# Optimization experiments

Measured on AMD Instinct MI355X. Metric: run time of the kernel, lower is better.

The kernel has to match this reference:

```python
import jax, jax.numpy as jnp
import numpy as np

C = 512
HEADS = 4
GROUPS = 32
EPS = 1e-6


def setup_inputs() -> dict:
    key = jax.random.key(0)
    ks = jax.random.split(key, 6)
    s = 1.0 / np.sqrt(C)
    return {
        "x": jax.random.normal(ks[0], (2, C, 64, 64), dtype=jnp.float32),
        "gn_scale": jnp.ones((C,), jnp.float32),
        "gn_bias": jnp.zeros((C,), jnp.float32),
        "wq": jax.random.normal(ks[1], (C, C), jnp.float32) * s,
        "bq": jnp.zeros((C,), jnp.float32),
        "wk": jax.random.normal(ks[2], (C, C), jnp.float32) * s,
        "bk": jnp.zeros((C,), jnp.float32),
        "wv": jax.random.normal(ks[3], (C, C), jnp.float32) * s,
        "bv": jnp.zeros((C,), jnp.float32),
        "wo": jax.random.normal(ks[4], (C, C), jnp.float32) * s,
        "bo": jnp.zeros((C,), jnp.float32),
    }


def group_norm(x, scale, bias):
    # x: [b, c, h, w]; GroupNorm with 32 groups, eps 1e-6, affine
    b, c, h, w = x.shape
    xg = x.reshape(b, GROUPS, c // GROUPS, h, w)
    mean = jnp.mean(xg, axis=(2, 3, 4), keepdims=True)
    var = jnp.var(xg, axis=(2, 3, 4), keepdims=True)
    xg = (xg - mean) * jax.lax.rsqrt(var + EPS)
    x = xg.reshape(b, c, h, w)
    return x * scale[None, :, None, None] + bias[None, :, None, None]


def conv1x1(x, w, b):
    # 1x1 conv == per-pixel linear: [b,c,h,w] x [o,c] -> [b,o,h,w]
    return jnp.einsum('bchw,oc->bohw', x, w) + b[None, :, None, None]


def reference(x, gn_scale, gn_bias, wq, bq, wk, bk, wv, bv, wo, bo):
    b, c, h, w = x.shape
    hc = c // HEADS
    n = h * w

    h_ = group_norm(x, gn_scale, gn_bias)
    q = conv1x1(h_, wq, bq).reshape(b, HEADS, hc, n)
    k = conv1x1(h_, wk, bk).reshape(b, HEADS, hc, n)
    v = conv1x1(h_, wv, bv).reshape(b, HEADS, hc, n)

    # NOTE: scale uses full channel count c (repo quirk), not head_channel
    scale = jnp.asarray(c, x.dtype) ** -0.5
    scores = jnp.einsum('bhcn,bhcm->bhnm', q, k) * scale  # [b,H,N,N]
    attn = jax.nn.softmax(scores, axis=-1)
    out = jnp.einsum('bhnm,bhcm->bhcn', attn, v)  # [b,H,hc,N]

    out = out.reshape(b, c, h, w)
    return x + conv1x1(out, wo, bo)
```

## Files before the change

### kernel.cpp

```cpp
#include <hip/hip_runtime.h>

typedef float    f32x4 __attribute__((ext_vector_type(4)));
typedef short    bf16x8 __attribute__((ext_vector_type(8)));
typedef unsigned short u16;
typedef u16      u16x4 __attribute__((ext_vector_type(4)));
typedef unsigned u32;
typedef u32      u32x4 __attribute__((ext_vector_type(4)));

#define MFMA16(a, b, c) __builtin_amdgcn_mfma_f32_16x16x32_bf16((a), (b), (c), 0, 0, 0)

#define CCH 512
#define NPIX 4096
#define NHEAD 4
#define HC 128
#define NSPLIT 2
#define KVCHUNK (NPIX / NSPLIT)
#define QK_SCALE 0.04419417382415922f
#define LOG2E 1.4426950408889634f

__device__ __forceinline__ u16 f2b(float f) {
  unsigned u = __builtin_bit_cast(unsigned, f);
  u += 0x7FFFu + ((u >> 16) & 1u);
  return (u16)(u >> 16);
}
__device__ __forceinline__ float b2f(u16 b) {
  return __builtin_bit_cast(float, ((unsigned)b) << 16);
}

__device__ __forceinline__ void gl_lds16(const u16* g, u16* l) {
  __builtin_amdgcn_global_load_lds((const __attribute__((address_space(1))) void*)g,
                                   (__attribute__((address_space(3))) void*)l, 16, 0, 0);
}

__global__ void prep_k(const float* __restrict__ w0, const float* __restrict__ w1,
                       const float* __restrict__ w2, const float* __restrict__ w3,
                       u16* __restrict__ dst,
                       const float* __restrict__ x, float* __restrict__ pstats) {
  int blk = blockIdx.x, t = threadIdx.x;
  if (blk < 1024) {
    int m = blk >> 8;
    const float* src = (m == 0) ? w0 : (m == 1) ? w1 : (m == 2) ? w2 : w3;
    int i = ((blk & 255) * 256 + t) * 4;
    f32x4 v = *(const f32x4*)(src + i);
    u16x4 o = { f2b(v[0]), f2b(v[1]), f2b(v[2]), f2b(v[3]) };
    *(u16x4*)(dst + (size_t)m * (CCH * CCH) + i) = o;
    return;
  }
  int sblk = blk - 1024;
  const f32x4* p = (const f32x4*)(x + (size_t)sblk * 4096);
  int wv = t >> 6, l = t & 63;
  float s = 0.f, ss = 0.f;
  #pragma unroll
  for (int i = t; i < 1024; i += 256) {
    f32x4 v = p[i];
    s  += v[0] + v[1] + v[2] + v[3];
    ss += v[0]*v[0] + v[1]*v[1] + v[2]*v[2] + v[3]*v[3];
  }
  #pragma unroll
  for (int d = 32; d; d >>= 1) { s += __shfl_down(s, d, 64); ss += __shfl_down(ss, d, 64); }
  __shared__ float red[8];
  if (l == 0) { red[wv*2] = s; red[wv*2+1] = ss; }
  __syncthreads();
  if (t == 0) {
    pstats[sblk*2]   = red[0] + red[2] + red[4] + red[6];
    pstats[sblk*2+1] = red[1] + red[3] + red[5] + red[7];
  }
}

__global__ void gn_norm_k(const float* __restrict__ x, const float* __restrict__ gns,
                          const float* __restrict__ gnb, const float* __restrict__ pstats,
                          u16* __restrict__ Ht) {
  int t = threadIdx.x;
  int ct = blockIdx.x * 64, nt = blockIdx.y * 64, b = blockIdx.z;
  int c0 = ct + (t & 15) * 4;
  int n0 = nt + (t >> 4) * 4;
  const float* xb = x + ((size_t)b * CCH + c0) * NPIX + n0;
  int g = b * 32 + (c0 >> 4);
  const f32x4* ps = (const f32x4*)(pstats + g * 32);
  float s = 0.f, ss = 0.f;
  #pragma unroll
  for (int j = 0; j < 8; ++j) {
    f32x4 v = ps[j];
    s  += v[0] + v[2];
    ss += v[1] + v[3];
  }
  float mean = s * (1.f/65536.f);
  float var  = ss * (1.f/65536.f) - mean*mean;
  float rstd = rsqrtf(var + 1e-6f);
  f32x4 rows[4];
  #pragma unroll
  for (int j = 0; j < 4; ++j) {
    f32x4 v = *(const f32x4*)(xb + (size_t)j * NPIX);
    float a  = rstd * gns[c0 + j];
    float bb = gnb[c0 + j] - mean * a;
    rows[j] = v * a + bb;
  }
  #pragma unroll
  for (int i = 0; i < 4; ++i) {
    u16x4 o = { f2b(rows[0][i]), f2b(rows[1][i]), f2b(rows[2][i]), f2b(rows[3][i]) };
    *(u16x4*)(Ht + ((size_t)b * NPIX + n0 + i) * CCH + c0) = o;
  }
}

template<int MODE>
__device__ __forceinline__ void gemm_body(const u16* __restrict__ A,
                                          const u16* __restrict__ B,
                                          const float* __restrict__ bias,
                                          const float* __restrict__ bias2,
                                          u16* __restrict__ outb,
                                          u16* __restrict__ outb2,
                                          float alpha,
                                          int bx, int by, int z,
                                          u16* As, u16* Bs) {
  const int t = threadIdx.x, l = t & 63, wv = t >> 6;
  const int l16 = l & 15, lq = l >> 4;
  const int mt = bx * 128, nt = by * 128;
  const u16* Ap = A + (size_t)mt * CCH;
  const u16* Bp = (MODE == 3) ? (B + (size_t)nt * CCH)
                              : (B + ((size_t)z * NPIX + nt) * CCH);
  const int wm = (wv >> 1) * 64, wn = (wv & 1) * 64;
  f32x4 acc[4][4] = {};

  #pragma unroll
  for (int j = 0; j < 2; ++j) {
    int idx = t + j * 256;
    int row = idx >> 2, kc = (idx & 3) * 8;
    gl_lds16(Ap + (size_t)row * CCH + kc, As + idx * 8);
    gl_lds16(Bp + (size_t)row * CCH + kc, Bs + idx * 8);
  }
  asm volatile("s_waitcnt vmcnt(0)" ::: "memory");
  __syncthreads();

#define GEMM_BODY(CUR, K0, DOSTAGE)                                                   \
  {                                                                                   \
    if (DOSTAGE) {                                                                    \
      _Pragma("unroll")                                                               \
      for (int j = 0; j < 2; ++j) {                                                   \
        int idx = t + j * 256;                                                        \
        int row = idx >> 2, kc = (idx & 3) * 8;                                       \
        gl_lds16(Ap + (size_t)row * CCH + (K0) + 32 + kc, As + ((CUR) ^ 1) * 4096 + idx * 8); \
        gl_lds16(Bp + (size_t)row * CCH + (K0) + 32 + kc, Bs + ((CUR) ^ 1) * 4096 + idx * 8); \
      }                                                                               \
    }                                                                                 \
    bf16x8 af[4], bfr[4];                                                             \
    _Pragma("unroll")                                                                 \
    for (int i = 0; i < 4; ++i) {                                                     \
      af[i]  = *(const bf16x8*)(As + (CUR) * 4096 + (wm + i * 16 + l16) * 32 + lq * 8); \
      bfr[i] = *(const bf16x8*)(Bs + (CUR) * 4096 + (wn + i * 16 + l16) * 32 + lq * 8); \
    }                                                                                 \
    _Pragma("unroll")                                                                 \
    for (int mi = 0; mi < 4; ++mi)                                                    \
      _Pragma("unroll")                                                               \
      for (int ni = 0; ni < 4; ++ni)                                                  \
        acc[mi][ni] = MFMA16(af[mi], bfr[ni], acc[mi][ni]);                           \
    asm volatile("s_waitcnt vmcnt(0)" ::: "memory");                                  \
    __syncthreads();                                                                  \
  }

  for (int k0 = 0; k0 < CCH; k0 += 64) {
    GEMM_BODY(0, k0, true)
    GEMM_BODY(1, k0 + 32, (k0 + 64 < CCH))
  }
#undef GEMM_BODY

  #pragma unroll
  for (int mi = 0; mi < 4; ++mi)
    #pragma unroll
    for (int ni = 0; ni < 4; ++ni)
      #pragma unroll
      for (int r = 0; r < 4; ++r) {
        int grow = mt + wm + mi * 16 + lq * 4 + r;
        int gcol = nt + wn + ni * 16 + l16;
        float v = acc[mi][ni][r];
        if (MODE == 1) {
          outb[((size_t)z * CCH + grow) * NPIX + gcol] = f2b(v + bias[grow]);
        } else {
          if (gcol < 512)
            outb[(size_t)grow * CCH + gcol] = f2b((v + bias[gcol]) * alpha);
          else
            outb2[(size_t)grow * CCH + (gcol - 512)] = f2b(v + bias2[gcol - 512]);
        }
      }
}

__global__ __launch_bounds__(256) void qkv_k(const u16* __restrict__ Ht,
                                             const u16* __restrict__ wb,
                                             const float* __restrict__ bq,
                                             const float* __restrict__ bk,
                                             const float* __restrict__ bv,
                                             u16* __restrict__ Qt, u16* __restrict__ Kt,
                                             u16* __restrict__ Vc, float alpha) {
  __shared__ __align__(16) u16 As[2][4096];
  __shared__ __align__(16) u16 Bs[2][4096];
  int blk = blockIdx.x;
  if (blk < 512) {
    gemm_body<3>(Ht, wb, bq, bk, Qt, Kt, alpha, blk & 63, blk >> 6, 0,
                 &As[0][0], &Bs[0][0]);
  } else {
    int r = blk - 512;
    gemm_body<1>(wb + 2u * 262144u, Ht, bv, nullptr, Vc, nullptr, 1.0f,
                 r & 3, (r >> 2) & 31, r >> 7, &As[0][0], &Bs[0][0]);
  }
}

__global__ __launch_bounds__(256, 2) void flash_k(const u16* __restrict__ Qt,
                                                  const u16* __restrict__ Kt,
                                                  const u16* __restrict__ Vc,
                                                  u16* __restrict__ sl0, u16* __restrict__ sl1,
                                                  float* __restrict__ mlp) {
  __shared__ __align__(16) char lds[65536];
  const int t = threadIdx.x, wv = t >> 6, l = t & 63;
  const int l16 = l & 15, lq = l >> 4;
  const int orig = blockIdx.x;
  const int gid = (orig & 7) * 64 + (orig >> 3);
  const int qx = gid & 31, grp = gid >> 5;
  const int hd = grp & 3, b = (grp >> 2) & 1, s = grp >> 3;
  const int qt0 = qx * 128 + wv * 32;

  const u16* Q = Qt + ((size_t)b * NPIX + qt0) * CCH + hd * HC;
  const u16* Kbase = Kt + (size_t)b * NPIX * CCH + hd * HC;
  const u16* Vbase = Vc + (size_t)b * CCH * NPIX + (size_t)hd * HC * NPIX;
  u16* slab = (s == 0) ? sl0 : sl1;
  u16* Ob = slab + ((size_t)(b * NHEAD + hd) * NPIX + qt0) * HC;
  size_t mlR0 = (size_t)s * 32768 + (size_t)(b * NHEAD + hd) * NPIX + qt0;

  bf16x8 qf[2][4];
  #pragma unroll
  for (int mi = 0; mi < 2; ++mi)
    #pragma unroll
    for (int kk = 0; kk < 4; ++kk)
      qf[mi][kk] = *(const bf16x8*)(Q + (size_t)(mi * 16 + l16) * CCH + kk * 32 + lq * 8);

  const int m_beg = s * KVCHUNK;
  const int sw = (l16 & 7) << 4;
  const int vb2 = (lq & 1) * 32 + (lq >> 1) * 16;

  int kbase[4], vbase[2];
  #pragma unroll
  for (int kk = 0; kk < 4; ++kk) kbase[kk] = l16 * 256 + ((kk * 64 + lq * 16) ^ sw);
  #pragma unroll
  for (int ks = 0; ks < 2; ++ks) vbase[ks] = 32768 + l16 * 128 + ((ks * 64 + vb2) ^ sw);

  u32 kgo[4], vgo[4];
  #pragma unroll
  for (int j = 0; j < 4; ++j) {
    int g = j * 256 + t;
    { int row = g >> 4, src = ((g & 15) << 4) ^ ((row & 7) << 4);
      kgo[j] = (u32)row * CCH + (src >> 1); }
    { int row = g >> 3, src = ((g & 7) << 4) ^ ((row & 7) << 4);
      vgo[j] = (u32)row * NPIX + (src >> 1); }
  }

  const short one_bf = (short)0x3F80;
  const bf16x8 vones = { one_bf, one_bf, one_bf, one_bf, one_bf, one_bf, one_bf, one_bf };

  f32x4 oacc[2][8] = {};
  f32x4 osum[2] = {};

  {
    const u16* kg = Kbase + (size_t)m_beg * CCH;
    const u16* vg = Vbase + m_beg;
    #pragma unroll
    for (int j = 0; j < 4; ++j) {
      gl_lds16(kg + kgo[j], (u16*)lds + (j * 256 + t) * 8);
      gl_lds16(vg + vgo[j], (u16*)(lds + 32768) + (j * 256 + t) * 8);
    }
  }
  asm volatile("s_waitcnt vmcnt(0)" ::: "memory");
  __syncthreads();

  const int NT = KVCHUNK / 64;

#define FLASH_BODY(CUR, M0, DOSTAGE)                                                   \
  {                                                                                    \
    if (DOSTAGE) {                                                                     \
      const u16* kg = Kbase + (size_t)((M0) + 64) * CCH;                               \
      const u16* vg = Vbase + ((M0) + 64);                                             \
      _Pragma("unroll")                                                                \
      for (int j = 0; j < 4; ++j) {                                                    \
        gl_lds16(kg + kgo[j], (u16*)(lds + ((CUR) ^ 1) * 16384) + (j * 256 + t) * 8);  \
        gl_lds16(vg + vgo[j], (u16*)(lds + 32768 + ((CUR) ^ 1) * 16384) + (j * 256 + t) * 8); \
      }                                                                                \
    }                                                                                  \
    f32x4 S[2][4] = {};                                                                \
    __builtin_amdgcn_s_setprio(1);                                                     \
    _Pragma("unroll")                                                                  \
    for (int kk = 0; kk < 4; ++kk)                                                     \
      _Pragma("unroll")                                                                \
      for (int mm = 0; mm < 4; ++mm) {                                                 \
        bf16x8 kf = *(const bf16x8*)(lds + kbase[kk] + mm * 4096 + (CUR) * 16384);     \
        S[0][mm] = MFMA16(kf, qf[0][kk], S[0][mm]);                                    \
        S[1][mm] = MFMA16(kf, qf[1][kk], S[1][mm]);                                    \
      }                                                                                \
    __builtin_amdgcn_s_setprio(0);                                                     \
    u32 pk[2][4][2];                                                                   \
    _Pragma("unroll")                                                                  \
    for (int mi = 0; mi < 2; ++mi) {                                                   \
      _Pragma("unroll")                                                                \
      for (int mm = 0; mm < 4; ++mm) {                                                 \
        f32x4 p;                                                                       \
        _Pragma("unroll")                                                              \
        for (int r = 0; r < 4; ++r) p[r] = exp2f(S[mi][mm][r]);                        \
        asm("v_cvt_pk_bf16_f32 %0, %1, %2" : "=v"(pk[mi][mm][0]) : "v"(p[0]), "v"(p[1])); \
        asm("v_cvt_pk_bf16_f32 %0, %1, %2" : "=v"(pk[mi][mm][1]) : "v"(p[2]), "v"(p[3])); \
      }                                                                                \
    }                                                                                  \
    bf16x8 pa[2][2];                                                                   \
    _Pragma("unroll")                                                                  \
    for (int mi = 0; mi < 2; ++mi)                                                     \
      _Pragma("unroll")                                                                \
      for (int ks = 0; ks < 2; ++ks) {                                                 \
        u32 a0 = pk[mi][2 * ks][0], a1 = pk[mi][2 * ks][1];                            \
        u32 b0 = pk[mi][2 * ks + 1][0], b1 = pk[mi][2 * ks + 1][1];                    \
        asm("v_permlane16_swap_b32 %0, %1" : "+v"(a0), "+v"(b0));                      \
        asm("v_permlane16_swap_b32 %0, %1" : "+v"(a1), "+v"(b1));                      \
        u32x4 w = { a0, a1, b0, b1 };                                                  \
        pa[mi][ks] = __builtin_bit_cast(bf16x8, w);                                    \
      }                                                                                \
    __builtin_amdgcn_s_setprio(1);                                                     \
    _Pragma("unroll")                                                                  \
    for (int ks = 0; ks < 2; ++ks) {                                                   \
      osum[0] = MFMA16(pa[0][ks], vones, osum[0]);                                     \
      osum[1] = MFMA16(pa[1][ks], vones, osum[1]);                                     \
      _Pragma("unroll")                                                                \
      for (int cc = 0; cc < 8; ++cc) {                                                 \
        bf16x8 vf = *(const bf16x8*)(lds + vbase[ks] + cc * 2048 + (CUR) * 16384);     \
        oacc[0][cc] = MFMA16(pa[0][ks], vf, oacc[0][cc]);                              \
        oacc[1][cc] = MFMA16(pa[1][ks], vf, oacc[1][cc]);                              \
      }                                                                                \
    }                                                                                  \
    __builtin_amdgcn_s_setprio(0);                                                     \
    asm volatile("s_waitcnt vmcnt(0)" ::: "memory");                                   \
    __syncthreads();                                                                   \
  }

  for (int it = 0; it < NT; it += 2) {
    FLASH_BODY(0, m_beg + it * 64, true)
    FLASH_BODY(1, m_beg + it * 64 + 64, (it + 2 < NT))
  }
#undef FLASH_BODY

  #pragma unroll
  for (int mi = 0; mi < 2; ++mi)
    #pragma unroll
    for (int cc = 0; cc < 8; ++cc)
      #pragma unroll
      for (int r = 0; r < 4; ++r)
        Ob[(size_t)(mi * 16 + lq * 4 + r) * HC + cc * 16 + l16] = f2b(oacc[mi][cc][r]);
  if (l16 == 0) {
    #pragma unroll
    for (int mi = 0; mi < 2; ++mi)
      #pragma unroll
      for (int r = 0; r < 4; ++r)
        mlp[mlR0 + mi * 16 + lq * 4 + r] = osum[mi][r];
  }
}

__global__ __launch_bounds__(256) void fgemm_k(const u16* __restrict__ Wo,
                                               const u16* __restrict__ sl0,
                                               const u16* __restrict__ sl1,
                                               const float* __restrict__ ml,
                                               const float* __restrict__ bias,
                                               const float* __restrict__ resid,
                                               float* __restrict__ outf) {
  __shared__ __align__(16) u16 As[2][4096];
  __shared__ __align__(16) u16 B0[2][2048];
  __shared__ __align__(16) u16 B1[2][2048];
  const int t = threadIdx.x, l = t & 63, wv = t >> 6;
  const int l16 = l & 15, lq = l >> 4;
  const int mt = blockIdx.x * 128, nt = blockIdx.y * 64, z = blockIdx.z;
  const u16* Ap = Wo + (size_t)mt * CCH;
  const int wm = (wv >> 1) * 64, wn = (wv & 1) * 32;

  float lsum[4][2];
  #pragma unroll
  for (int h = 0; h < 4; ++h)
    #pragma unroll
    for (int ni = 0; ni < 2; ++ni) {
      int gcol = nt + wn + ni * 16 + l16;
      int R = ((z * 4 + h) << 12) + gcol;
      lsum[h][ni] = ml[R] + ml[32768 + R];
    }

  f32x4 acc[4][2] = {};

  #pragma unroll
  for (int j = 0; j < 2; ++j) {
    int idx = t + j * 256;
    int row = idx >> 2, kc = (idx & 3) * 8;
    gl_lds16(Ap + (size_t)row * CCH + kc, &As[0][0] + idx * 8);
  }
  {
    int row = t >> 2, kc = (t & 3) * 8;
    size_t srow = ((size_t)(z * 4) * NPIX + nt + row) * HC + kc;
    gl_lds16(sl0 + srow, &B0[0][0] + t * 8);
    gl_lds16(sl1 + srow, &B1[0][0] + t * 8);
  }
  asm volatile("s_waitcnt vmcnt(0)" ::: "memory");
  __syncthreads();

#define FG_BODY(CUR, K0, DOSTAGE)                                                     \
  {                                                                                   \
    if (DOSTAGE) {                                                                    \
      const int kn = (K0) + 32;                                                       \
      const int hn = kn >> 7, cn = kn & 127;                                          \
      _Pragma("unroll")                                                               \
      for (int j = 0; j < 2; ++j) {                                                   \
        int idx = t + j * 256;                                                        \
        int row = idx >> 2, kc = (idx & 3) * 8;                                       \
        gl_lds16(Ap + (size_t)row * CCH + kn + kc, &As[(CUR) ^ 1][0] + idx * 8);      \
      }                                                                               \
      {                                                                               \
        int row = t >> 2, kc = (t & 3) * 8;                                           \
        size_t srow = ((size_t)(z * 4 + hn) * NPIX + nt + row) * HC + cn + kc;        \
        gl_lds16(sl0 + srow, &B0[(CUR) ^ 1][0] + t * 8);                              \
        gl_lds16(sl1 + srow, &B1[(CUR) ^ 1][0] + t * 8);                              \
      }                                                                               \
    }                                                                                 \
    bf16x8 af[4], b0f[2], b1f[2];                                                     \
    _Pragma("unroll")                                                                 \
    for (int i = 0; i < 4; ++i)                                                       \
      af[i]  = *(const bf16x8*)(&As[CUR][0] + (wm + i * 16 + l16) * 32 + lq * 8);     \
    _Pragma("unroll")                                                                 \
    for (int i = 0; i < 2; ++i) {                                                     \
      b0f[i] = *(const bf16x8*)(&B0[CUR][0] + (wn + i * 16 + l16) * 32 + lq * 8);     \
      b1f[i] = *(const bf16x8*)(&B1[CUR][0] + (wn + i * 16 + l16) * 32 + lq * 8);     \
    }                                                                                 \
    _Pragma("unroll")                                                                 \
    for (int mi = 0; mi < 4; ++mi)                                                    \
      _Pragma("unroll")                                                               \
      for (int ni = 0; ni < 2; ++ni) {                                                \
        acc[mi][ni] = MFMA16(af[mi], b0f[ni], acc[mi][ni]);                           \
        acc[mi][ni] = MFMA16(af[mi], b1f[ni], acc[mi][ni]);                           \
      }                                                                               \
    asm volatile("s_waitcnt vmcnt(0)" ::: "memory");                                  \
    __syncthreads();                                                                  \
  }

  #pragma unroll
  for (int h = 0; h < 4; ++h) {
    if (h) {
      #pragma unroll
      for (int ni = 0; ni < 2; ++ni) {
        float rat = lsum[h][ni] / lsum[h - 1][ni];
        #pragma unroll
        for (int mi = 0; mi < 4; ++mi) acc[mi][ni] *= rat;
      }
    }
    FG_BODY(0, h * 128,      true)
    FG_BODY(1, h * 128 + 32, true)
    FG_BODY(0, h * 128 + 64, true)
    FG_BODY(1, h * 128 + 96, (h < 3))
  }
#undef FG_BODY

  #pragma unroll
  for (int ni = 0; ni < 2; ++ni) {
    float inv3 = 1.f / lsum[3][ni];
    int gcol = nt + wn + ni * 16 + l16;
    #pragma unroll
    for (int mi = 0; mi < 4; ++mi)
      #pragma unroll
      for (int r = 0; r < 4; ++r) {
        int grow = mt + wm + mi * 16 + lq * 4 + r;
        size_t off = ((size_t)z * CCH + grow) * NPIX + gcol;
        outf[off] = acc[mi][ni][r] * inv3 + bias[grow] + resid[off];
      }
  }
}

extern "C" void kernel_launch(void* const* d_in, const int* in_sizes, int n_in,
                              void* d_out, int out_size, void* d_ws, size_t ws_size,
                              hipStream_t stream) {
  const float* x   = (const float*)d_in[0];
  const float* gns = (const float*)d_in[1];
  const float* gnb = (const float*)d_in[2];
  const float* wq  = (const float*)d_in[3];
  const float* bq  = (const float*)d_in[4];
  const float* wk  = (const float*)d_in[5];
  const float* bk  = (const float*)d_in[6];
  const float* wv  = (const float*)d_in[7];
  const float* bv  = (const float*)d_in[8];
  const float* wo  = (const float*)d_in[9];
  const float* bo  = (const float*)d_in[10];
  float* out = (float*)d_out;
  char* ws = (char*)d_ws;

  u16*   wb    = (u16*)ws;
  u16*   Ht    = (u16*)(ws + (size_t)( 2u << 20));
  u16*   Qt    = (u16*)(ws + (size_t)(10u << 20));
  u16*   Kt    = (u16*)(ws + (size_t)(18u << 20));
  u16*   Vc    = (u16*)(ws + (size_t)(26u << 20));
  u16*   sl1   = (u16*)(ws + (size_t)(34u << 20));
  float* mlb   = (float*)(ws + (size_t)(42u << 20));
  float* stats = (float*)(ws + (size_t)(43u << 20));
  u16*   sl0   = Ht;

  prep_k    <<<dim3(2048, 1, 1), 256, 0, stream>>>(wq, wk, wv, wo, wb, x, stats);
  gn_norm_k <<<dim3(8, 64, 2),   256, 0, stream>>>(x, gns, gnb, stats, Ht);
  qkv_k     <<<dim3(768, 1, 1),  256, 0, stream>>>(Ht, wb, bq, bk, bv, Qt, Kt, Vc,
                                                   QK_SCALE * LOG2E);
  flash_k   <<<dim3(512, 1, 1),  256, 0, stream>>>(Qt, Kt, Vc, sl0, sl1, mlb);
  fgemm_k   <<<dim3(4, 64, 2),   256, 0, stream>>>(wb + 3u * 262144u, sl0, sl1, mlb,
                                                   bo, x, out);
}
```

Before: 143.1 us.

## Halve QKV GEMM N-tile and flash KV tile to shrink LDS and raise occupancy

The QKV GEMM tile shrinks from 128x128 to 128x64, doubling the grid to 1536 blocks and halving B-side shared memory. The flash attention kernel's KV tile drops from 64 to 32 keys per iteration, halving LDS to 32KB and adjusting the V swizzle and permlane packing to a single k-step. The intent is better occupancy and wave-level parallelism. The cost is more loop iterations with barrier overhead and less operand reuse per tile.

After: 147.9 us. 1.03x slower.

```diff
diff --git a/kernel.cpp b/kernel.cpp
--- a/kernel.cpp
+++ b/kernel.cpp
@@ -114,19 +114,22 @@
                                           u16* As, u16* Bs) {
   const int t = threadIdx.x, l = t & 63, wv = t >> 6;
   const int l16 = l & 15, lq = l >> 4;
-  const int mt = bx * 128, nt = by * 128;
+  const int mt = bx * 128, nt = by * 64;
   const u16* Ap = A + (size_t)mt * CCH;
   const u16* Bp = (MODE == 3) ? (B + (size_t)nt * CCH)
                               : (B + ((size_t)z * NPIX + nt) * CCH);
-  const int wm = (wv >> 1) * 64, wn = (wv & 1) * 64;
-  f32x4 acc[4][4] = {};
+  const int wm = (wv >> 1) * 64, wn = (wv & 1) * 32;
+  f32x4 acc[4][2] = {};
 
   #pragma unroll
   for (int j = 0; j < 2; ++j) {
     int idx = t + j * 256;
     int row = idx >> 2, kc = (idx & 3) * 8;
     gl_lds16(Ap + (size_t)row * CCH + kc, As + idx * 8);
-    gl_lds16(Bp + (size_t)row * CCH + kc, Bs + idx * 8);
+  }
+  {
+    int row = t >> 2, kc = (t & 3) * 8;
+    gl_lds16(Bp + (size_t)row * CCH + kc, Bs + t * 8);
   }
   asm volatile("s_waitcnt vmcnt(0)" ::: "memory");
   __syncthreads();
@@ -139,19 +142,23 @@
         int idx = t + j * 256;                                                        \
         int row = idx >> 2, kc = (idx & 3) * 8;                                       \
         gl_lds16(Ap + (size_t)row * CCH + (K0) + 32 + kc, As + ((CUR) ^ 1) * 4096 + idx * 8); \
-        gl_lds16(Bp + (size_t)row * CCH + (K0) + 32 + kc, Bs + ((CUR) ^ 1) * 4096 + idx * 8); \
+      }                                                                               \
+      {                                                                               \
+        int row = t >> 2, kc = (t & 3) * 8;                                           \
+        gl_lds16(Bp + (size_t)row * CCH + (K0) + 32 + kc, Bs + ((CUR) ^ 1) * 2048 + t * 8); \
       }                                                                               \
     }                                                                                 \
-    bf16x8 af[4], bfr[4];                                                             \
+    bf16x8 af[4], bfr[2];                                                             \
     _Pragma("unroll")                                                                 \
-    for (int i = 0; i < 4; ++i) {                                                     \
+    for (int i = 0; i < 4; ++i)                                                       \
       af[i]  = *(const bf16x8*)(As + (CUR) * 4096 + (wm + i * 16 + l16) * 32 + lq * 8); \
-      bfr[i] = *(const bf16x8*)(Bs + (CUR) * 4096 + (wn + i * 16 + l16) * 32 + lq * 8); \
-    }                                                                                 \
+    _Pragma("unroll")                                                                 \
+    for (int i = 0; i < 2; ++i)                                                       \
+      bfr[i] = *(const bf16x8*)(Bs + (CUR) * 2048 + (wn + i * 16 + l16) * 32 + lq * 8); \
     _Pragma("unroll")                                                                 \
     for (int mi = 0; mi < 4; ++mi)                                                    \
       _Pragma("unroll")                                                               \
-      for (int ni = 0; ni < 4; ++ni)                                                  \
+      for (int ni = 0; ni < 2; ++ni)                                                  \
         acc[mi][ni] = MFMA16(af[mi], bfr[ni], acc[mi][ni]);                           \
     asm volatile("s_waitcnt vmcnt(0)" ::: "memory");                                  \
     __syncthreads();                                                                  \
@@ -166,7 +173,7 @@
   #pragma unroll
   for (int mi = 0; mi < 4; ++mi)
     #pragma unroll
-    for (int ni = 0; ni < 4; ++ni)
+    for (int ni = 0; ni < 2; ++ni)
       #pragma unroll
       for (int r = 0; r < 4; ++r) {
         int grow = mt + wm + mi * 16 + lq * 4 + r;
@@ -191,15 +198,15 @@
                                              u16* __restrict__ Qt, u16* __restrict__ Kt,
                                              u16* __restrict__ Vc, float alpha) {
   __shared__ __align__(16) u16 As[2][4096];
-  __shared__ __align__(16) u16 Bs[2][4096];
+  __shared__ __align__(16) u16 Bs[2][2048];
   int blk = blockIdx.x;
-  if (blk < 512) {
-    gemm_body<3>(Ht, wb, bq, bk, Qt, Kt, alpha, blk & 63, blk >> 6, 0,
+  if (blk < 1024) {
+    gemm_body<3>(Ht, wb, bq, bk, Qt, Kt, alpha, blk >> 4, blk & 15, 0,
                  &As[0][0], &Bs[0][0]);
   } else {
-    int r = blk - 512;
+    int r = blk - 1024;
     gemm_body<1>(wb + 2u * 262144u, Ht, bv, nullptr, Vc, nullptr, 1.0f,
-                 r & 3, (r >> 2) & 31, r >> 7, &As[0][0], &Bs[0][0]);
+                 r & 3, (r >> 2) & 63, r >> 8, &As[0][0], &Bs[0][0]);
   }
 }
 
@@ -208,7 +215,7 @@
                                                   const u16* __restrict__ Vc,
                                                   u16* __restrict__ sl0, u16* __restrict__ sl1,
                                                   float* __restrict__ mlp) {
-  __shared__ __align__(16) char lds[65536];
+  __shared__ __align__(16) char lds[32768];
   const int t = threadIdx.x, wv = t >> 6, l = t & 63;
   const int l16 = l & 15, lq = l >> 4;
   const int orig = blockIdx.x;
@@ -232,22 +239,21 @@
       qf[mi][kk] = *(const bf16x8*)(Q + (size_t)(mi * 16 + l16) * CCH + kk * 32 + lq * 8);
 
   const int m_beg = s * KVCHUNK;
-  const int sw = (l16 & 7) << 4;
   const int vb2 = (lq & 1) * 32 + (lq >> 1) * 16;
 
-  int kbase[4], vbase[2];
-  #pragma unroll
-  for (int kk = 0; kk < 4; ++kk) kbase[kk] = l16 * 256 + ((kk * 64 + lq * 16) ^ sw);
-  #pragma unroll
-  for (int ks = 0; ks < 2; ++ks) vbase[ks] = 32768 + l16 * 128 + ((ks * 64 + vb2) ^ sw);
-
-  u32 kgo[4], vgo[4];
-  #pragma unroll
-  for (int j = 0; j < 4; ++j) {
+  int kbase[4];
+  #pragma unroll
+  for (int kk = 0; kk < 4; ++kk)
+    kbase[kk] = l16 * 256 + ((kk * 64 + lq * 16) ^ ((l16 & 7) << 4));
+  const int vbase = 16384 + l16 * 64 + (vb2 ^ ((l16 & 3) << 4));
+
+  u32 kgo[2], vgo[2];
+  #pragma unroll
+  for (int j = 0; j < 2; ++j) {
     int g = j * 256 + t;
     { int row = g >> 4, src = ((g & 15) << 4) ^ ((row & 7) << 4);
       kgo[j] = (u32)row * CCH + (src >> 1); }
-    { int row = g >> 3, src = ((g & 7) << 4) ^ ((row & 7) << 4);
+    { int row = g >> 2, src = ((g & 3) << 4) ^ ((row & 3) << 4);
       vgo[j] = (u32)row * NPIX + (src >> 1); }
   }
 
@@ -261,43 +267,43 @@
     const u16* kg = Kbase + (size_t)m_beg * CCH;
     const u16* vg = Vbase + m_beg;
     #pragma unroll
-    for (int j = 0; j < 4; ++j) {
+    for (int j = 0; j < 2; ++j) {
       gl_lds16(kg + kgo[j], (u16*)lds + (j * 256 + t) * 8);
-      gl_lds16(vg + vgo[j], (u16*)(lds + 32768) + (j * 256 + t) * 8);
+      gl_lds16(vg + vgo[j], (u16*)(lds + 16384) + (j * 256 + t) * 8);
     }
   }
   asm volatile("s_waitcnt vmcnt(0)" ::: "memory");
   __syncthreads();
 
-  const int NT = KVCHUNK / 64;
+  const int NT = KVCHUNK / 32;
 
 #define FLASH_BODY(CUR, M0, DOSTAGE)                                                   \
   {                                                                                    \
     if (DOSTAGE) {                                                                     \
-      const u16* kg = Kbase + (size_t)((M0) + 64) * CCH;                               \
-      const u16* vg = Vbase + ((M0) + 64);                                             \
+      const u16* kg = Kbase + (size_t)((M0) + 32) * CCH;                               \
+      const u16* vg = Vbase + ((M0) + 32);                                             \
       _Pragma("unroll")                                                                \
-      for (int j = 0; j < 4; ++j) {                                                    \
-        gl_lds16(kg + kgo[j], (u16*)(lds + ((CUR) ^ 1) * 16384) + (j * 256 + t) * 8);  \
-        gl_lds16(vg + vgo[j], (u16*)(lds + 32768 + ((CUR) ^ 1) * 16384) + (j * 256 + t) * 8); \
+      for (int j = 0; j < 2; ++j) {                                                    \
+        gl_lds16(kg + kgo[j], (u16*)(lds + ((CUR) ^ 1) * 8192) + (j * 256 + t) * 8);   \
+        gl_lds16(vg + vgo[j], (u16*)(lds + 16384 + ((CUR) ^ 1) * 8192) + (j * 256 + t) * 8); \
       }                                                                                \
     }                                                                                  \
-    f32x4 S[2][4] = {};                                                                \
+    f32x4 S[2][2] = {};                                                                \
     __builtin_amdgcn_s_setprio(1);                                                     \
     _Pragma("unroll")                                                                  \
     for (int kk = 0; kk < 4; ++kk)                                                     \
       _Pragma("unroll")                                                                \
-      for (int mm = 0; mm < 4; ++mm) {                                                 \
-        bf16x8 kf = *(const bf16x8*)(lds + kbase[kk] + mm * 4096 + (CUR) * 16384);     \
+      for (int mm = 0; mm < 2; ++mm) {                                                 \
+        bf16x8 kf = *(const bf16x8*)(lds + kbase[kk] + mm * 4096 + (CUR) * 8192);      \
         S[0][mm] = MFMA16(kf, qf[0][kk], S[0][mm]);                                    \
         S[1][mm] = MFMA16(kf, qf[1][kk], S[1][mm]);                                    \
       }                                                                                \
     __builtin_amdgcn_s_setprio(0);                                                     \
-    u32 pk[2][4][2];                                                                   \
+    u32 pk[2][2][2];                                                                   \
     _Pragma("unroll")                                                                  \
     for (int mi = 0; mi < 2; ++mi) {                                                   \
       _Pragma("unroll")                                                                \
-      for (int mm = 0; mm < 4; ++mm) {                                                 \
+      for (int mm = 0; mm < 2; ++mm) {                                                 \
         f32x4 p;                                                                       \
         _Pragma("unroll")                                                              \
         for (int r = 0; r < 4; ++r) p[r] = exp2f(S[mi][mm][r]);                        \
@@ -305,29 +311,24 @@
         asm("v_cvt_pk_bf16_f32 %0, %1, %2" : "=v"(pk[mi][mm][1]) : "v"(p[2]), "v"(p[3])); \
       }                                                                                \
     }                                                                                  \
-    bf16x8 pa[2][2];                                                                   \
+    bf16x8 pa[2];                                                                      \
     _Pragma("unroll")                                                                  \
-    for (int mi = 0; mi < 2; ++mi)                                                     \
-      _Pragma("unroll")                                                                \
-      for (int ks = 0; ks < 2; ++ks) {                                                 \
-        u32 a0 = pk[mi][2 * ks][0], a1 = pk[mi][2 * ks][1];                            \
-        u32 b0 = pk[mi][2 * ks + 1][0], b1 = pk[mi][2 * ks + 1][1];                    \
-        asm("v_permlane16_swap_b32 %0, %1" : "+v"(a0), "+v"(b0));                      \
-        asm("v_permlane16_swap_b32 %0, %1" : "+v"(a1), "+v"(b1));                      \
-        u32x4 w = { a0, a1, b0, b1 };                                                  \
-        pa[mi][ks] = __builtin_bit_cast(bf16x8, w);                                    \
-      }                                                                                \
+    for (int mi = 0; mi < 2; ++mi) {                                                   \
+      u32 a0 = pk[mi][0][0], a1 = pk[mi][0][1];                                        \
+      u32 b0 = pk[mi][1][0], b1 = pk[mi][1][1];                                        \
+      asm("v_permlane16_swap_b32 %0, %1" : "+v"(a0), "+v"(b0));                        \
+      asm("v_permlane16_swap_b32 %0, %1" : "+v"(a1), "+v"(b1));                        \
+      u32x4 w = { a0, a1, b0, b1 };                                                    \
+      pa[mi] = __builtin_bit_cast(bf16x8, w);                                          \
+    }                                                                                  \
     __builtin_amdgcn_s_setprio(1);                                                     \
+    osum[0] = MFMA16(pa[0], vones, osum[0]);                                           \
+    osum[1] = MFMA16(pa[1], vones, osum[1]);                                           \
     _Pragma("unroll")                                                                  \
-    for (int ks = 0; ks < 2; ++ks) {                                                   \
-      osum[0] = MFMA16(pa[0][ks], vones, osum[0]);                                     \
-      osum[1] = MFMA16(pa[1][ks], vones, osum[1]);                                     \
-      _Pragma("unroll")                                                                \
-      for (int cc = 0; cc < 8; ++cc) {                                                 \
-        bf16x8 vf = *(const bf16x8*)(lds + vbase[ks] + cc * 2048 + (CUR) * 16384);     \
-        oacc[0][cc] = MFMA16(pa[0][ks], vf, oacc[0][cc]);                              \
-        oacc[1][cc] = MFMA16(pa[1][ks], vf, oacc[1][cc]);                              \
-      }                                                                                \
+    for (int cc = 0; cc < 8; ++cc) {                                                   \
+      bf16x8 vf = *(const bf16x8*)(lds + vbase + cc * 1024 + (CUR) * 8192);            \
+      oacc[0][cc] = MFMA16(pa[0], vf, oacc[0][cc]);                                    \
+      oacc[1][cc] = MFMA16(pa[1], vf, oacc[1][cc]);                                    \
     }                                                                                  \
     __builtin_amdgcn_s_setprio(0);                                                     \
     asm volatile("s_waitcnt vmcnt(0)" ::: "memory");                                   \
@@ -335,8 +336,8 @@
   }
 
   for (int it = 0; it < NT; it += 2) {
-    FLASH_BODY(0, m_beg + it * 64, true)
-    FLASH_BODY(1, m_beg + it * 64 + 64, (it + 2 < NT))
+    FLASH_BODY(0, m_beg + it * 32, true)
+    FLASH_BODY(1, m_beg + it * 32 + 32, (it + 2 < NT))
   }
 #undef FLASH_BODY
 
@@ -498,7 +499,7 @@
 
   prep_k    <<<dim3(2048, 1, 1), 256, 0, stream>>>(wq, wk, wv, wo, wb, x, stats);
   gn_norm_k <<<dim3(8, 64, 2),   256, 0, stream>>>(x, gns, gnb, stats, Ht);
-  qkv_k     <<<dim3(768, 1, 1),  256, 0, stream>>>(Ht, wb, bq, bk, bv, Qt, Kt, Vc,
+  qkv_k     <<<dim3(1536, 1, 1), 256, 0, stream>>>(Ht, wb, bq, bk, bv, Qt, Kt, Vc,
                                                    QK_SCALE * LOG2E);
   flash_k   <<<dim3(512, 1, 1),  256, 0, stream>>>(Qt, Kt, Vc, sl0, sl1, mlb);
   fgemm_k   <<<dim3(4, 64, 2),   256, 0, stream>>>(wb + 3u * 262144u, sl0, sl1, mlb,
```
